# Kernel optimization log

Hardware: AMD Instinct MI355X
Metric: run time of the kernel (lower is better)

Reference implementation:

```python
import jax, jax.numpy as jnp
import numpy as np

N = 200000
E = 5000000


def _gcn_norm(edge_index, num_nodes):
    # add self-loops and compute symmetric normalization (PyG GCNConv default)
    loop = jnp.arange(num_nodes, dtype=edge_index.dtype)
    src = jnp.concatenate([edge_index[0], loop])
    dst = jnp.concatenate([edge_index[1], loop])
    ones = jnp.ones(dst.shape[0], dtype=jnp.float32)
    deg = jax.ops.segment_sum(ones, dst, num_segments=num_nodes)
    dis = jnp.where(deg > 0, jax.lax.rsqrt(deg), 0.0)
    norm = dis[src] * dis[dst]  # [E+N]
    return src, dst, norm


def _gcn_layer(x, src, dst, norm, W, b, num_nodes):
    xl = x @ W  # [N, out] dense linear (no bias, PyG default)
    msg = xl[src] * norm[:, None]  # gather + scale
    agg = jax.ops.segment_sum(msg, dst, num_segments=num_nodes)  # scatter-add
    return agg + b


def setup_inputs() -> dict:
    key = jax.random.key(0)
    ks = jax.random.split(key, 10)
    x = jax.random.normal(ks[0], (N, 12), dtype=jnp.float32)
    edge_index = jax.random.randint(ks[1], (2, E), 0, N, dtype=jnp.int64)
    def glorot(k, fi, fo):
        s = np.sqrt(6.0 / (fi + fo)).astype(np.float32)
        return jax.random.uniform(k, (fi, fo), jnp.float32, -s, s)
    return {
        "x": x,
        "edge_index": edge_index,
        "W1": glorot(ks[2], 12, 16), "b1": jnp.zeros((16,), jnp.float32),
        "W2": glorot(ks[3], 16, 8), "b2": jnp.zeros((8,), jnp.float32),
        "W3": glorot(ks[4], 8, 16), "b3": jnp.zeros((16,), jnp.float32),
        "W4": glorot(ks[5], 16, 12), "b4": jnp.zeros((12,), jnp.float32),
    }


def reference(x, edge_index, W1, b1, W2, b2, W3, b3, W4, b4):
    num_nodes = x.shape[0]
    src, dst, norm = _gcn_norm(edge_index, num_nodes)
    # Encoder
    h = jax.nn.relu(_gcn_layer(x, src, dst, norm, W1, b1, num_nodes))
    h = _gcn_layer(h, src, dst, norm, W2, b2, num_nodes)
    # Decoder
    h = jax.nn.relu(_gcn_layer(h, src, dst, norm, W3, b3, num_nodes))
    h = jax.nn.sigmoid(_gcn_layer(h, src, dst, norm, W4, b4, num_nodes))
    return h
```

## Files before the change

kernel.cpp:

```cpp
#include <hip/hip_runtime.h>
#include <hip/hip_fp16.h>
#include <math.h>


#define NPB 1024
#define MAX_NB 256
#define CAP 26496
#define BIN_CHUNK 4096
#define BIN_TH 512
#define EPT (BIN_CHUNK / BIN_TH)
#define MAXB CAP

__global__ void init_cur_kernel(int* __restrict__ bucket_cur, int NB) {
    int t = blockIdx.x * blockDim.x + threadIdx.x;
    if (t < NB) bucket_cur[t] = t * CAP;
}

__global__ __launch_bounds__(BIN_TH) void bin_kernel(const int* __restrict__ src,
                                                     const int* __restrict__ dst,
                                                     int* __restrict__ bucket_cur,
                                                     unsigned int* __restrict__ binned,
                                                     int E, int NB) {
    __shared__ int h[MAX_NB];
    __shared__ int scl[MAX_NB + 1];
    __shared__ int base[MAX_NB];
    __shared__ int sscan[256];
    __shared__ unsigned int stage[BIN_CHUNK];
    __shared__ unsigned char bkt8[BIN_CHUNK];
    int cbeg = blockIdx.x * BIN_CHUNK;
    int cend = min(cbeg + BIN_CHUNK, E);
    int chunk_n = cend - cbeg;
    int tid = threadIdx.x;

    for (int t = tid; t < NB; t += BIN_TH) h[t] = 0;
    __syncthreads();
    int myd[EPT];
#pragma unroll
    for (int j = 0; j < EPT; j++) {
        int e = cbeg + tid + j * BIN_TH;
        if (e < cend) {
            myd[j] = dst[e];
            atomicAdd(&h[myd[j] >> 10], 1);
        }
    }
    __syncthreads();
    int v = (tid < NB) ? h[tid] : 0;
    if (tid < 256) sscan[tid] = v;
    __syncthreads();
    for (int off = 1; off < 256; off <<= 1) {
        int t = (tid >= off && tid < 256) ? sscan[tid - off] : 0;
        __syncthreads();
        if (tid < 256) sscan[tid] += t;
        __syncthreads();
    }
    if (tid < NB) {
        scl[tid] = sscan[tid] - v;
        base[tid] = v ? atomicAdd(&bucket_cur[tid], v) : 0;
    }
    if (tid == 0) scl[NB] = chunk_n;
    __syncthreads();
    for (int t = tid; t < NB; t += BIN_TH) h[t] = 0;
    __syncthreads();
#pragma unroll
    for (int j = 0; j < EPT; j++) {
        int e = cbeg + tid + j * BIN_TH;
        if (e < cend) {
            int d = myd[j];
            int bkt = d >> 10;
            int pos = scl[bkt] + atomicAdd(&h[bkt], 1);
            stage[pos] = ((unsigned)src[e] << 10) | (unsigned)(d & 1023);
            bkt8[pos] = (unsigned char)bkt;
        }
    }
    __syncthreads();
    for (int k = tid; k < chunk_n; k += BIN_TH) {
        int bkt = bkt8[k];
        binned[base[bkt] + (k - scl[bkt])] = stage[k];
    }
}

__global__ __launch_bounds__(1024) void csr_bucket_t1_kernel(
    const unsigned int* __restrict__ binned,
    const int* __restrict__ bucket_cur,
    int2* __restrict__ rows, float* __restrict__ dis,
    int* __restrict__ col,
    const float* __restrict__ x,
    __half* __restrict__ xls, int N) {
    __shared__ int cnt[NPB];
    __shared__ int cur[NPB];
    __shared__ int colbuf[MAXB];
    int b = blockIdx.x;
    int nbase = b << 10;
    int nlocal = min(NPB, N - nbase);
    int beg = b * CAP;
    int bsize = bucket_cur[b] - beg;
    int tid = threadIdx.x;

    cnt[tid] = 0;
    __syncthreads();
    for (int k = tid; k < bsize; k += 1024)
        atomicAdd(&cnt[binned[beg + k] & 1023u], 1);
    __syncthreads();
    int v = cnt[tid];
    cur[tid] = v;
    __syncthreads();
    for (int off = 1; off < 1024; off <<= 1) {
        int t = (tid >= off) ? cur[tid - off] : 0;
        __syncthreads();
        cur[tid] += t;
        __syncthreads();
    }
    int excl = cur[tid] - v;
    float d = 1.0f / sqrtf((float)(v + 1));
    if (tid < nlocal) {
        rows[nbase + tid] = make_int2(beg + excl, beg + excl + v);
        dis[nbase + tid] = d;
    }
    __syncthreads();
    cur[tid] = excl;
    __syncthreads();
    if (bsize <= MAXB) {
        for (int k = tid; k < bsize; k += 1024) {
            unsigned rec = binned[beg + k];
            int pos = atomicAdd(&cur[rec & 1023u], 1);
            colbuf[pos] = (int)(rec >> 10);
        }
        __syncthreads();
        for (int k = tid; k < bsize; k += 1024) col[beg + k] = colbuf[k];
    } else {
        for (int k = tid; k < bsize; k += 1024) {
            unsigned rec = binned[beg + k];
            int pos = atomicAdd(&cur[rec & 1023u], 1);
            col[beg + pos] = (int)(rec >> 10);
        }
    }
    if (tid < nlocal) {
        int i = nbase + tid;
        float h[12];
#pragma unroll
        for (int k = 0; k < 12; k++) h[k] = x[(size_t)i * 12 + k];
        __half2* x2 = (__half2*)xls;
#pragma unroll
        for (int k = 0; k < 6; k++) {
            x2[(size_t)i * 6 + k] =
                __floats2half2_rn(h[2 * k] * d, h[2 * k + 1] * d);
        }
    }
}

template <int P>
__device__ __forceinline__ void acc_node(const __half2* __restrict__ x2, int c,
                                         float2 (&acc)[P]) {
    __half2 t[P];
#pragma unroll
    for (int k = 0; k < P; k++) t[k] = x2[(size_t)c * P + k];
#pragma unroll
    for (int k = 0; k < P; k++) {
        float2 v = __half22float2(t[k]);
        acc[k].x += v.x;
        acc[k].y += v.y;
    }
}

template <int P>
__device__ __forceinline__ void acc_quad(const __half2* __restrict__ x2, int4 c,
                                         float2 (&acc)[P]) {
    __half2 t[4][P];
#pragma unroll
    for (int k = 0; k < P; k++) t[0][k] = x2[(size_t)c.x * P + k];
#pragma unroll
    for (int k = 0; k < P; k++) t[1][k] = x2[(size_t)c.y * P + k];
#pragma unroll
    for (int k = 0; k < P; k++) t[2][k] = x2[(size_t)c.z * P + k];
#pragma unroll
    for (int k = 0; k < P; k++) t[3][k] = x2[(size_t)c.w * P + k];
#pragma unroll
    for (int k = 0; k < P; k++) {
        float2 a0 = __half22float2(t[0][k]), a1 = __half22float2(t[1][k]);
        float2 a2 = __half22float2(t[2][k]), a3 = __half22float2(t[3][k]);
        acc[k].x += (a0.x + a1.x) + (a2.x + a3.x);
        acc[k].y += (a0.y + a1.y) + (a2.y + a3.y);
    }
}

template <int C>
__device__ __forceinline__ void gather_acc(
    int i, int p, const int2* __restrict__ rows, const int* __restrict__ col,
    const __half2* __restrict__ x2, float2 (&acc)[C / 2]) {
    constexpr int P = C / 2;
    constexpr int UN = (P >= 6) ? 2 : 3;
#pragma unroll
    for (int k = 0; k < P; k++) {
        if (p == 0) acc[k] = __half22float2(x2[(size_t)i * P + k]);
        else acc[k] = make_float2(0.0f, 0.0f);
    }
    int2 r = rows[i];
    int beg = r.x;
    int end = r.y;
    int nedge = end - beg;
    int pre = (4 - (beg & 3)) & 3;
    if (pre > nedge) pre = nedge;
    for (int j = p; j < pre; j += 2) acc_node<P>(x2, col[beg + j], acc);
    int abeg = beg + pre;
    int nq = (end - abeg) >> 2;
    int q = p;
    for (; q + 2 * (UN - 1) < nq; q += 2 * UN) {
        int4 cs[UN];
#pragma unroll
        for (int u = 0; u < UN; u++)
            cs[u] = *reinterpret_cast<const int4*>(col + abeg + 4 * (q + 2 * u));
#pragma unroll
        for (int u = 0; u < UN; u++) acc_quad<P>(x2, cs[u], acc);
    }
    for (; q < nq; q += 2) {
        int4 ca = *reinterpret_cast<const int4*>(col + abeg + 4 * q);
        acc_quad<P>(x2, ca, acc);
    }
    int tbeg = abeg + 4 * nq;
    for (int j = tbeg + p; j < end; j += 2) acc_node<P>(x2, col[j], acc);
#pragma unroll
    for (int k = 0; k < P; k++) {
        acc[k].x += __shfl_xor(acc[k].x, 1);
        acc[k].y += __shfl_xor(acc[k].y, 1);
    }
}

__global__ __launch_bounds__(256) void gather12_kernel(
    const int2* __restrict__ rows, const int* __restrict__ col,
    const float* __restrict__ dis, const __half* __restrict__ xin,
    float* __restrict__ agg, int N) {
    int tid = blockIdx.x * blockDim.x + threadIdx.x;
    int i = tid >> 1;
    int p = tid & 1;
    if (i >= N) return;
    float2 acc[6];
    gather_acc<12>(i, p, rows, col, (const __half2*)xin, acc);
    float d = dis[i];
    float2* ap = (float2*)(agg + (size_t)i * 12);
#pragma unroll
    for (int k = 0; k < 6; k++) {
        if ((k & 1) == p) ap[k] = make_float2(acc[k].x * d, acc[k].y * d);
    }
}

__global__ __launch_bounds__(256) void transform12_kernel(
    const float* __restrict__ a0,
    const float* __restrict__ b1, const float* __restrict__ W1,
    const float* __restrict__ W2, const float* __restrict__ dis,
    __half* __restrict__ xout, int N) {
    __shared__ float sW1[12 * 16];
    __shared__ float sW2[16 * 8];
    __shared__ float sB[16];
    if (threadIdx.x < 192) sW1[threadIdx.x] = W1[threadIdx.x];
    if (threadIdx.x < 128) sW2[threadIdx.x] = W2[threadIdx.x];
    if (threadIdx.x < 16) sB[threadIdx.x] = b1[threadIdx.x];
    __syncthreads();
    int i = blockIdx.x * blockDim.x + threadIdx.x;
    if (i >= N) return;
    float A[12];
#pragma unroll
    for (int k = 0; k < 12; k++) A[k] = a0[(size_t)i * 12 + k];
    float h[16];
#pragma unroll
    for (int f = 0; f < 16; f++) {
        float acc = sB[f];
#pragma unroll
        for (int k = 0; k < 12; k++) acc = fmaf(A[k], sW1[k * 16 + f], acc);
        h[f] = fmaxf(acc, 0.0f);
    }
    float d = dis[i];
    __half2* x2 = (__half2*)xout;
#pragma unroll
    for (int k2 = 0; k2 < 4; k2++) {
        float o0 = 0.0f, o1 = 0.0f;
#pragma unroll
        for (int k = 0; k < 16; k++) {
            o0 = fmaf(h[k], sW2[k * 8 + 2 * k2], o0);
            o1 = fmaf(h[k], sW2[k * 8 + 2 * k2 + 1], o1);
        }
        x2[(size_t)i * 4 + k2] = __floats2half2_rn(o0 * d, o1 * d);
    }
}

__global__ __launch_bounds__(256) void gather8_t3_kernel(
    const int2* __restrict__ rows, const int* __restrict__ col,
    const float* __restrict__ dis, const __half* __restrict__ xin,
    const float* __restrict__ b2, __half* __restrict__ xout, int N) {
    int tid = blockIdx.x * blockDim.x + threadIdx.x;
    int i = tid >> 1;
    int p = tid & 1;
    if (i >= N) return;
    float2 acc[4];
    gather_acc<8>(i, p, rows, col, (const __half2*)xin, acc);
    float d = dis[i];
    __half2* x2o = (__half2*)xout;
#pragma unroll
    for (int k = 0; k < 4; k++) {
        if ((k >> 1) == p) {
            x2o[(size_t)i * 4 + k] =
                __floats2half2_rn((acc[k].x * d + b2[2 * k]) * d,
                                  (acc[k].y * d + b2[2 * k + 1]) * d);
        }
    }
}

__global__ __launch_bounds__(256) void gather8_t4_kernel(
    const int2* __restrict__ rows, const int* __restrict__ col,
    const float* __restrict__ dis, const __half* __restrict__ xin,
    const float* __restrict__ b3, const float* __restrict__ W3,
    const float* __restrict__ W4, __half* __restrict__ xout, int N) {
    __shared__ float sW3[8 * 16];
    __shared__ float sW4[16 * 12];
    __shared__ float sB[16];
    if (threadIdx.x < 128) sW3[threadIdx.x] = W3[threadIdx.x];
    if (threadIdx.x < 192) sW4[threadIdx.x] = W4[threadIdx.x];
    if (threadIdx.x < 16) sB[threadIdx.x] = b3[threadIdx.x];
    __syncthreads();
    int tid = blockIdx.x * blockDim.x + threadIdx.x;
    int i = tid >> 1;
    int p = tid & 1;
    if (i >= N) return;
    float2 acc[4];
    gather_acc<8>(i, p, rows, col, (const __half2*)xin, acc);
    float d = dis[i];
    float A[8];
#pragma unroll
    for (int k = 0; k < 4; k++) {
        A[2 * k] = acc[k].x * d;
        A[2 * k + 1] = acc[k].y * d;
    }
    float h[8];
#pragma unroll
    for (int f = 0; f < 8; f++) {
        float a = sB[p * 8 + f];
#pragma unroll
        for (int k = 0; k < 8; k++) a = fmaf(A[k], sW3[k * 16 + p * 8 + f], a);
        h[f] = fmaxf(a, 0.0f);
    }
    float o[12];
#pragma unroll
    for (int j = 0; j < 12; j++) {
        float a = 0.0f;
#pragma unroll
        for (int f = 0; f < 8; f++) a = fmaf(h[f], sW4[(p * 8 + f) * 12 + j], a);
        o[j] = a;
    }
#pragma unroll
    for (int j = 0; j < 12; j++) o[j] += __shfl_xor(o[j], 1);
    __half2* x2o = (__half2*)xout;
#pragma unroll
    for (int k = 0; k < 3; k++) {
        x2o[(size_t)i * 6 + p * 3 + k] =
            __floats2half2_rn(o[6 * p + 2 * k] * d, o[6 * p + 2 * k + 1] * d);
    }
}

__global__ __launch_bounds__(256) void gather12_sig_kernel(
    const int2* __restrict__ rows, const int* __restrict__ col,
    const float* __restrict__ dis, const __half* __restrict__ xin,
    const float* __restrict__ bias, float* __restrict__ out, int N) {
    int tid = blockIdx.x * blockDim.x + threadIdx.x;
    int i = tid >> 1;
    int p = tid & 1;
    if (i >= N) return;
    float2 acc[6];
    gather_acc<12>(i, p, rows, col, (const __half2*)xin, acc);
    float d = dis[i];
    float* op = out + (size_t)i * 12;
#pragma unroll
    for (int k = 0; k < 6; k++) {
        if ((k & 1) == p) {
            float vx = 1.0f / (1.0f + expf(-(acc[k].x * d + bias[2 * k])));
            float vy = 1.0f / (1.0f + expf(-(acc[k].y * d + bias[2 * k + 1])));
            *reinterpret_cast<float2*>(op + 2 * k) = make_float2(vx, vy);
        }
    }
}

static inline size_t align_up(size_t v, size_t a) { return (v + a - 1) & ~(a - 1); }

extern "C" void kernel_launch(void* const* d_in, const int* in_sizes, int n_in,
                              void* d_out, int out_size, void* d_ws, size_t ws_size,
                              hipStream_t stream) {
    const float* x  = (const float*)d_in[0];
    const int*   ei = (const int*)d_in[1];
    const float* W1 = (const float*)d_in[2];
    const float* b1 = (const float*)d_in[3];
    const float* W2 = (const float*)d_in[4];
    const float* b2 = (const float*)d_in[5];
    const float* W3 = (const float*)d_in[6];
    const float* b3 = (const float*)d_in[7];
    const float* W4 = (const float*)d_in[8];
    const float* b4 = (const float*)d_in[9];
    float* out = (float*)d_out;

    const int N = in_sizes[0] / 12;
    const int E = in_sizes[1] / 2;
    const int* src = ei;
    const int* dst = ei + E;
    const int NB = (N + NPB - 1) / NPB;

    char* ws = (char*)d_ws;
    size_t off = 0;
    int* bucket_cur = (int*)(ws + off);   off = align_up(off + (size_t)NB * 4, 256);
    int2* rows = (int2*)(ws + off);       off = align_up(off + (size_t)N * 8, 256);
    float* dis = (float*)(ws + off);      off = align_up(off + (size_t)N * 4, 256);
    unsigned int* binned = (unsigned int*)(ws + off);
    off = align_up(off + ((size_t)NB * CAP + 4096) * 4, 256);
    int* col = (int*)(ws + off);          off = align_up(off + ((size_t)NB * CAP + 4096) * 4, 256);
    __half* xls = (__half*)(ws + off);    off = align_up(off + (size_t)N * 16 * 2, 256);
    __half* xls2 = (__half*)(ws + off);   off = align_up(off + (size_t)N * 16 * 2, 256);
    float* aggA = (float*)(ws + off);     off = align_up(off + (size_t)N * 12 * 4, 256);
    (void)ws_size; (void)n_in; (void)out_size;

    const int B = 256;
    auto blocks = [&](long long n) { return (int)((n + B - 1) / B); };

    init_cur_kernel<<<1, 256, 0, stream>>>(bucket_cur, NB);
    bin_kernel<<<(E + BIN_CHUNK - 1) / BIN_CHUNK, BIN_TH, 0, stream>>>(src, dst, bucket_cur, binned, E, NB);
    csr_bucket_t1_kernel<<<NB, 1024, 0, stream>>>(binned, bucket_cur, rows, dis, col,
                                                  x, xls, N);

    gather12_kernel<<<blocks(2LL * N), B, 0, stream>>>(rows, col, dis, xls, aggA, N);

    transform12_kernel<<<blocks(N), B, 0, stream>>>(aggA, b1, W1, W2, dis, xls2, N);

    gather8_t3_kernel<<<blocks(2LL * N), B, 0, stream>>>(rows, col, dis, xls2, b2, xls, N);

    gather8_t4_kernel<<<blocks(2LL * N), B, 0, stream>>>(rows, col, dis, xls, b3, W3, W4,
                                                         xls2, N);

    gather12_sig_kernel<<<blocks(2LL * N), B, 0, stream>>>(rows, col, dis, xls2, b4, out, N);
}
```

Baseline: 371.7 us.

## Split 12-channel gathers by source-half to improve cache locality

After: 360.4 us. 3.0% less time.

```diff
diff --git a/kernel.cpp b/kernel.cpp
--- a/kernel.cpp
+++ b/kernel.cpp
@@ -82,12 +82,14 @@
 __global__ __launch_bounds__(1024) void csr_bucket_t1_kernel(
     const unsigned int* __restrict__ binned,
     const int* __restrict__ bucket_cur,
-    int2* __restrict__ rows, float* __restrict__ dis,
+    int2* __restrict__ rows, int* __restrict__ mids, float* __restrict__ dis,
     int* __restrict__ col,
     const float* __restrict__ x,
-    __half* __restrict__ xls, int N) {
+    __half* __restrict__ xls, int N, int halfN) {
     __shared__ int cnt[NPB];
-    __shared__ int cur[NPB];
+    __shared__ int cnt0[NPB];
+    __shared__ int curA[NPB];
+    __shared__ int curB[NPB];
     __shared__ int colbuf[MAXB];
     int b = blockIdx.x;
     int nbase = b << 10;
@@ -97,41 +99,56 @@
     int tid = threadIdx.x;
 
     cnt[tid] = 0;
-    __syncthreads();
-    for (int k = tid; k < bsize; k += 1024)
-        atomicAdd(&cnt[binned[beg + k] & 1023u], 1);
+    cnt0[tid] = 0;
+    __syncthreads();
+    for (int k = tid; k < bsize; k += 1024) {
+        unsigned rec = binned[beg + k];
+        int l = rec & 1023u;
+        int s = (int)(rec >> 10);
+        atomicAdd(&cnt[l], 1);
+        if (s < halfN) atomicAdd(&cnt0[l], 1);
+    }
     __syncthreads();
     int v = cnt[tid];
-    cur[tid] = v;
+    int v0 = cnt0[tid];
+    curA[tid] = v;
     __syncthreads();
     for (int off = 1; off < 1024; off <<= 1) {
-        int t = (tid >= off) ? cur[tid - off] : 0;
+        int t = (tid >= off) ? curA[tid - off] : 0;
         __syncthreads();
-        cur[tid] += t;
+        curA[tid] += t;
         __syncthreads();
     }
-    int excl = cur[tid] - v;
+    int excl = curA[tid] - v;
     float d = 1.0f / sqrtf((float)(v + 1));
     if (tid < nlocal) {
         rows[nbase + tid] = make_int2(beg + excl, beg + excl + v);
+        mids[nbase + tid] = beg + excl + v0;
         dis[nbase + tid] = d;
     }
     __syncthreads();
-    cur[tid] = excl;
+    curA[tid] = excl;
+    curB[tid] = excl + v0;
     __syncthreads();
     if (bsize <= MAXB) {
         for (int k = tid; k < bsize; k += 1024) {
             unsigned rec = binned[beg + k];
-            int pos = atomicAdd(&cur[rec & 1023u], 1);
-            colbuf[pos] = (int)(rec >> 10);
+            int l = rec & 1023u;
+            int s = (int)(rec >> 10);
+            int pos = (s < halfN) ? atomicAdd(&curA[l], 1)
+                                  : atomicAdd(&curB[l], 1);
+            colbuf[pos] = s;
         }
         __syncthreads();
         for (int k = tid; k < bsize; k += 1024) col[beg + k] = colbuf[k];
     } else {
         for (int k = tid; k < bsize; k += 1024) {
             unsigned rec = binned[beg + k];
-            int pos = atomicAdd(&cur[rec & 1023u], 1);
-            col[beg + pos] = (int)(rec >> 10);
+            int l = rec & 1023u;
+            int s = (int)(rec >> 10);
+            int pos = (s < halfN) ? atomicAdd(&curA[l], 1)
+                                  : atomicAdd(&curB[l], 1);
+            col[beg + pos] = s;
         }
     }
     if (tid < nlocal) {
@@ -142,18 +159,18 @@
         __half2* x2 = (__half2*)xls;
 #pragma unroll
         for (int k = 0; k < 6; k++) {
-            x2[(size_t)i * 6 + k] =
+            x2[(size_t)i * 8 + k] =
                 __floats2half2_rn(h[2 * k] * d, h[2 * k + 1] * d);
         }
     }
 }
 
-template <int P>
+template <int P, int S>
 __device__ __forceinline__ void acc_node(const __half2* __restrict__ x2, int c,
                                          float2 (&acc)[P]) {
     __half2 t[P];
 #pragma unroll
-    for (int k = 0; k < P; k++) t[k] = x2[(size_t)c * P + k];
+    for (int k = 0; k < P; k++) t[k] = x2[(size_t)c * S + k];
 #pragma unroll
     for (int k = 0; k < P; k++) {
         float2 v = __half22float2(t[k]);
@@ -162,18 +179,18 @@
     }
 }
 
-template <int P>
+template <int P, int S>
 __device__ __forceinline__ void acc_quad(const __half2* __restrict__ x2, int4 c,
                                          float2 (&acc)[P]) {
     __half2 t[4][P];
 #pragma unroll
-    for (int k = 0; k < P; k++) t[0][k] = x2[(size_t)c.x * P + k];
-#pragma unroll
-    for (int k = 0; k < P; k++) t[1][k] = x2[(size_t)c.y * P + k];
-#pragma unroll
-    for (int k = 0; k < P; k++) t[2][k] = x2[(size_t)c.z * P + k];
-#pragma unroll
-    for (int k = 0; k < P; k++) t[3][k] = x2[(size_t)c.w * P + k];
+    for (int k = 0; k < P; k++) t[0][k] = x2[(size_t)c.x * S + k];
+#pragma unroll
+    for (int k = 0; k < P; k++) t[1][k] = x2[(size_t)c.y * S + k];
+#pragma unroll
+    for (int k = 0; k < P; k++) t[2][k] = x2[(size_t)c.z * S + k];
+#pragma unroll
+    for (int k = 0; k < P; k++) t[3][k] = x2[(size_t)c.w * S + k];
 #pragma unroll
     for (int k = 0; k < P; k++) {
         float2 a0 = __half22float2(t[0][k]), a1 = __half22float2(t[1][k]);
@@ -183,24 +200,22 @@
     }
 }
 
-template <int C>
-__device__ __forceinline__ void gather_acc(
-    int i, int p, const int2* __restrict__ rows, const int* __restrict__ col,
-    const __half2* __restrict__ x2, float2 (&acc)[C / 2]) {
+template <int C, int S>
+__device__ __forceinline__ void gather_acc_rng(
+    int i, int p, int beg, int end, bool self,
+    const int* __restrict__ col, const __half2* __restrict__ x2,
+    float2 (&acc)[C / 2]) {
     constexpr int P = C / 2;
     constexpr int UN = (P >= 6) ? 2 : 3;
 #pragma unroll
     for (int k = 0; k < P; k++) {
-        if (p == 0) acc[k] = __half22float2(x2[(size_t)i * P + k]);
+        if (self && p == 0) acc[k] = __half22float2(x2[(size_t)i * S + k]);
         else acc[k] = make_float2(0.0f, 0.0f);
     }
-    int2 r = rows[i];
-    int beg = r.x;
-    int end = r.y;
     int nedge = end - beg;
     int pre = (4 - (beg & 3)) & 3;
     if (pre > nedge) pre = nedge;
-    for (int j = p; j < pre; j += 2) acc_node<P>(x2, col[beg + j], acc);
+    for (int j = p; j < pre; j += 2) acc_node<P, S>(x2, col[beg + j], acc);
     int abeg = beg + pre;
     int nq = (end - abeg) >> 2;
     int q = p;
@@ -210,14 +225,14 @@
         for (int u = 0; u < UN; u++)
             cs[u] = *reinterpret_cast<const int4*>(col + abeg + 4 * (q + 2 * u));
 #pragma unroll
-        for (int u = 0; u < UN; u++) acc_quad<P>(x2, cs[u], acc);
+        for (int u = 0; u < UN; u++) acc_quad<P, S>(x2, cs[u], acc);
     }
     for (; q < nq; q += 2) {
         int4 ca = *reinterpret_cast<const int4*>(col + abeg + 4 * q);
-        acc_quad<P>(x2, ca, acc);
+        acc_quad<P, S>(x2, ca, acc);
     }
     int tbeg = abeg + 4 * nq;
-    for (int j = tbeg + p; j < end; j += 2) acc_node<P>(x2, col[j], acc);
+    for (int j = tbeg + p; j < end; j += 2) acc_node<P, S>(x2, col[j], acc);
 #pragma unroll
     for (int k = 0; k < P; k++) {
         acc[k].x += __shfl_xor(acc[k].x, 1);
@@ -225,26 +240,35 @@
     }
 }
 
-__global__ __launch_bounds__(256) void gather12_kernel(
-    const int2* __restrict__ rows, const int* __restrict__ col,
-    const float* __restrict__ dis, const __half* __restrict__ xin,
-    float* __restrict__ agg, int N) {
-    int tid = blockIdx.x * blockDim.x + threadIdx.x;
-    int i = tid >> 1;
-    int p = tid & 1;
+__global__ __launch_bounds__(256) void gather12h_kernel(
+    const int2* __restrict__ rows, const int* __restrict__ mids,
+    const int* __restrict__ col, const __half* __restrict__ xin,
+    float* __restrict__ part0, float* __restrict__ part1, int N, int halfN) {
+    int grp = blockIdx.x >> 3;
+    int sub = blockIdx.x & 7;
+    int chunk = sub >> 2;
+    int range = (grp << 2) + (sub & 3);
+    int t2 = range * 256 + (int)threadIdx.x;
+    int i = t2 >> 1;
+    int p = t2 & 1;
     if (i >= N) return;
+    int2 r = rows[i];
+    int m = mids[i];
+    int beg = chunk ? m : r.x;
+    int end = chunk ? r.y : m;
+    bool self = chunk ? (i >= halfN) : (i < halfN);
     float2 acc[6];
-    gather_acc<12>(i, p, rows, col, (const __half2*)xin, acc);
-    float d = dis[i];
-    float2* ap = (float2*)(agg + (size_t)i * 12);
+    gather_acc_rng<12, 8>(i, p, beg, end, self, col, (const __half2*)xin, acc);
+    float* part = chunk ? part1 : part0;
+    float2* ap = (float2*)(part + (size_t)i * 12);
 #pragma unroll
     for (int k = 0; k < 6; k++) {
-        if ((k & 1) == p) ap[k] = make_float2(acc[k].x * d, acc[k].y * d);
+        if ((k & 1) == p) ap[k] = acc[k];
     }
 }
 
 __global__ __launch_bounds__(256) void transform12_kernel(
-    const float* __restrict__ a0,
+    const float* __restrict__ p0, const float* __restrict__ p1,
     const float* __restrict__ b1, const float* __restrict__ W1,
     const float* __restrict__ W2, const float* __restrict__ dis,
     __half* __restrict__ xout, int N) {
@@ -257,9 +281,18 @@
     __syncthreads();
     int i = blockIdx.x * blockDim.x + threadIdx.x;
     if (i >= N) return;
+    float d = dis[i];
     float A[12];
-#pragma unroll
-    for (int k = 0; k < 12; k++) A[k] = a0[(size_t)i * 12 + k];
+    const float4* a4 = (const float4*)(p0 + (size_t)i * 12);
+    const float4* b4 = (const float4*)(p1 + (size_t)i * 12);
+#pragma unroll
+    for (int q = 0; q < 3; q++) {
+        float4 va = a4[q], vb = b4[q];
+        A[4 * q + 0] = (va.x + vb.x) * d;
+        A[4 * q + 1] = (va.y + vb.y) * d;
+        A[4 * q + 2] = (va.z + vb.z) * d;
+        A[4 * q + 3] = (va.w + vb.w) * d;
+    }
     float h[16];
 #pragma unroll
     for (int f = 0; f < 16; f++) {
@@ -268,7 +301,6 @@
         for (int k = 0; k < 12; k++) acc = fmaf(A[k], sW1[k * 16 + f], acc);
         h[f] = fmaxf(acc, 0.0f);
     }
-    float d = dis[i];
     __half2* x2 = (__half2*)xout;
 #pragma unroll
     for (int k2 = 0; k2 < 4; k2++) {
@@ -290,8 +322,9 @@
     int i = tid >> 1;
     int p = tid & 1;
     if (i >= N) return;
+    int2 r = rows[i];
     float2 acc[4];
-    gather_acc<8>(i, p, rows, col, (const __half2*)xin, acc);
+    gather_acc_rng<8, 4>(i, p, r.x, r.y, true, col, (const __half2*)xin, acc);
     float d = dis[i];
     __half2* x2o = (__half2*)xout;
 #pragma unroll
@@ -320,8 +353,9 @@
     int i = tid >> 1;
     int p = tid & 1;
     if (i >= N) return;
+    int2 r = rows[i];
     float2 acc[4];
-    gather_acc<8>(i, p, rows, col, (const __half2*)xin, acc);
+    gather_acc_rng<8, 4>(i, p, r.x, r.y, true, col, (const __half2*)xin, acc);
     float d = dis[i];
     float A[8];
 #pragma unroll
@@ -348,32 +382,43 @@
 #pragma unroll
     for (int j = 0; j < 12; j++) o[j] += __shfl_xor(o[j], 1);
     __half2* x2o = (__half2*)xout;
-#pragma unroll
-    for (int k = 0; k < 3; k++) {
-        x2o[(size_t)i * 6 + p * 3 + k] =
-            __floats2half2_rn(o[6 * p + 2 * k] * d, o[6 * p + 2 * k + 1] * d);
-    }
-}
-
-__global__ __launch_bounds__(256) void gather12_sig_kernel(
-    const int2* __restrict__ rows, const int* __restrict__ col,
-    const float* __restrict__ dis, const __half* __restrict__ xin,
-    const float* __restrict__ bias, float* __restrict__ out, int N) {
-    int tid = blockIdx.x * blockDim.x + threadIdx.x;
-    int i = tid >> 1;
-    int p = tid & 1;
+    if (p == 0) {
+#pragma unroll
+        for (int k = 0; k < 4; k++) {
+            x2o[(size_t)i * 8 + k] =
+                __floats2half2_rn(o[2 * k] * d, o[2 * k + 1] * d);
+        }
+    } else {
+#pragma unroll
+        for (int k = 0; k < 2; k++) {
+            x2o[(size_t)i * 8 + 4 + k] =
+                __floats2half2_rn(o[8 + 2 * k] * d, o[9 + 2 * k] * d);
+        }
+    }
+}
+
+__global__ __launch_bounds__(256) void combine_sig_kernel(
+    const float* __restrict__ p0, const float* __restrict__ p1,
+    const float* __restrict__ dis, const float* __restrict__ bias,
+    float* __restrict__ out, int N) {
+    __shared__ float sB[12];
+    if (threadIdx.x < 12) sB[threadIdx.x] = bias[threadIdx.x];
+    __syncthreads();
+    int i = blockIdx.x * blockDim.x + threadIdx.x;
     if (i >= N) return;
-    float2 acc[6];
-    gather_acc<12>(i, p, rows, col, (const __half2*)xin, acc);
     float d = dis[i];
-    float* op = out + (size_t)i * 12;
-#pragma unroll
-    for (int k = 0; k < 6; k++) {
-        if ((k & 1) == p) {
-            float vx = 1.0f / (1.0f + expf(-(acc[k].x * d + bias[2 * k])));
-            float vy = 1.0f / (1.0f + expf(-(acc[k].y * d + bias[2 * k + 1])));
-            *reinterpret_cast<float2*>(op + 2 * k) = make_float2(vx, vy);
-        }
+    const float4* a4 = (const float4*)(p0 + (size_t)i * 12);
+    const float4* b4 = (const float4*)(p1 + (size_t)i * 12);
+    float4* o4 = (float4*)(out + (size_t)i * 12);
+#pragma unroll
+    for (int q = 0; q < 3; q++) {
+        float4 va = a4[q], vb = b4[q];
+        float4 r;
+        r.x = 1.0f / (1.0f + expf(-((va.x + vb.x) * d + sB[4 * q + 0])));
+        r.y = 1.0f / (1.0f + expf(-((va.y + vb.y) * d + sB[4 * q + 1])));
+        r.z = 1.0f / (1.0f + expf(-((va.z + vb.z) * d + sB[4 * q + 2])));
+        r.w = 1.0f / (1.0f + expf(-((va.w + vb.w) * d + sB[4 * q + 3])));
+        o4[q] = r;
     }
 }
 
@@ -396,6 +441,7 @@
 
     const int N = in_sizes[0] / 12;
     const int E = in_sizes[1] / 2;
+    const int halfN = N >> 1;
     const int* src = ei;
     const int* dst = ei + E;
     const int NB = (N + NPB - 1) / NPB;
@@ -404,31 +450,39 @@
     size_t off = 0;
     int* bucket_cur = (int*)(ws + off);   off = align_up(off + (size_t)NB * 4, 256);
     int2* rows = (int2*)(ws + off);       off = align_up(off + (size_t)N * 8, 256);
+    int* mids = (int*)(ws + off);         off = align_up(off + (size_t)N * 4, 256);
     float* dis = (float*)(ws + off);      off = align_up(off + (size_t)N * 4, 256);
     unsigned int* binned = (unsigned int*)(ws + off);
     off = align_up(off + ((size_t)NB * CAP + 4096) * 4, 256);
     int* col = (int*)(ws + off);          off = align_up(off + ((size_t)NB * CAP + 4096) * 4, 256);
     __half* xls = (__half*)(ws + off);    off = align_up(off + (size_t)N * 16 * 2, 256);
     __half* xls2 = (__half*)(ws + off);   off = align_up(off + (size_t)N * 16 * 2, 256);
-    float* aggA = (float*)(ws + off);     off = align_up(off + (size_t)N * 12 * 4, 256);
     (void)ws_size; (void)n_in; (void)out_size;
+
+    float* part0 = (float*)binned;
+    float* part1 = part0 + (size_t)N * 12;
 
     const int B = 256;
     auto blocks = [&](long long n) { return (int)((n + B - 1) / B); };
+    int nb2 = blocks(2LL * N);
+    nb2 = (nb2 + 3) & ~3;
+    const int G2 = nb2 * 2;
 
     init_cur_kernel<<<1, 256, 0, stream>>>(bucket_cur, NB);
     bin_kernel<<<(E + BIN_CHUNK - 1) / BIN_CHUNK, BIN_TH, 0, stream>>>(src, dst, bucket_cur, binned, E, NB);
-    csr_bucket_t1_kernel<<<NB, 1024, 0, stream>>>(binned, bucket_cur, rows, dis, col,
-                                                  x, xls, N);
-
-    gather12_kernel<<<blocks(2LL * N), B, 0, stream>>>(rows, col, dis, xls, aggA, N);
-
-    transform12_kernel<<<blocks(N), B, 0, stream>>>(aggA, b1, W1, W2, dis, xls2, N);
+    csr_bucket_t1_kernel<<<NB, 1024, 0, stream>>>(binned, bucket_cur, rows, mids, dis,
+                                                  col, x, xls, N, halfN);
+
+    gather12h_kernel<<<G2, B, 0, stream>>>(rows, mids, col, xls, part0, part1, N, halfN);
+
+    transform12_kernel<<<blocks(N), B, 0, stream>>>(part0, part1, b1, W1, W2, dis, xls2, N);
 
     gather8_t3_kernel<<<blocks(2LL * N), B, 0, stream>>>(rows, col, dis, xls2, b2, xls, N);
 
     gather8_t4_kernel<<<blocks(2LL * N), B, 0, stream>>>(rows, col, dis, xls, b3, W3, W4,
                                                          xls2, N);
 
-    gather12_sig_kernel<<<blocks(2LL * N), B, 0, stream>>>(rows, col, dis, xls2, b4, out, N);
-}
+    gather12h_kernel<<<G2, B, 0, stream>>>(rows, mids, col, xls2, part0, part1, N, halfN);
+
+    combine_sig_kernel<<<blocks(N), B, 0, stream>>>(part0, part1, dis, b4, out, N);
+}
```
